# Performance work log

Hardware: AMD Instinct MI355X
Metric: run time of the kernel (lower is better)

Reference implementation:

```python
import jax, jax.numpy as jnp
import numpy as np

NLAG = 300  # int(maxlag/dt) = int(3.0/0.01)


def setup_inputs() -> dict:
    key = jax.random.key(0)
    k1, k2 = jax.random.split(key)
    data1 = jax.random.normal(k1, (64, 32, 3000), dtype=jnp.float32)
    data2 = jax.random.normal(k2, (64, 32, 3000), dtype=jnp.float32)
    return {"data1": data1, "data2": data2}


def reference(data1, data2):
    # Time-domain full cross-correlation via grouped conv1d (PyTorch conv1d
    # does correlation, no kernel flip; lax.conv_general_dilated matches).
    nb, nc, nt = data1.shape
    g = nb * nc
    lhs = data1.reshape(1, g, nt)          # (N=1, C=g, T)
    rhs = data2.reshape(g, 1, nt)          # (O=g, I=1, T) one filter per group
    xcor = jax.lax.conv_general_dilated(
        lhs, rhs,
        window_strides=(1,),
        padding=[(NLAG + 1, NLAG + 1)],
        feature_group_count=g,
        dimension_numbers=("NCH", "OIH", "NCH"),
    )  # (1, g, 2*NLAG+3)
    return xcor.reshape(nb, nc, -1)
```

## Files before the change

### kernel.cpp

```cpp
#include <hip/hip_runtime.h>


#define NT    3000
#define NOUT  603
#define CHPB  4
#define BLOCK 256

#define L1B  6784
#define L2B  8192
#define CHB  (L1B + L2B)
#define TOTB (CHB * CHPB)

typedef short bf16x8 __attribute__((ext_vector_type(8)));
typedef float f32x4  __attribute__((ext_vector_type(4)));

static __device__ __forceinline__ uint f2bf(float f) {
    union { float f; uint u; } a; a.f = f;
    return (a.u + 0x7fffu + ((a.u >> 16) & 1u)) >> 16;
}

__global__ __launch_bounds__(BLOCK, 2) void xcorr_mfma(
    const float* __restrict__ d1g, const float* __restrict__ d2g,
    float* __restrict__ out)
{
    __shared__ __align__(16) unsigned char smem[TOTB];
    const int tid = threadIdx.x;

    int4* z = (int4*)smem;
    for (int i = tid; i < TOTB / 16; i += BLOCK) z[i] = int4{0, 0, 0, 0};
    __syncthreads();

    const int chBase = blockIdx.x * CHPB;

    for (int i = tid; i < CHPB * 750; i += BLOCK) {
        const int c = i / 750, j = i % 750;
        const float4 v = *(const float4*)(d1g + (size_t)(chBase + c) * NT + 4 * j);
        uint2 p;
        p.x = f2bf(v.x) | (f2bf(v.y) << 16);
        p.y = f2bf(v.z) | (f2bf(v.w) << 16);
        *(uint2*)(smem + c * CHB + 608 + 8 * j) = p;
    }
    for (int i = tid; i < CHPB * 750; i += BLOCK) {
        const int c = i / 750, j = i % 750;
        const float4 v = *(const float4*)(d2g + (size_t)(chBase + c) * NT + 4 * j);
        uint2 p;
        p.x = f2bf(v.x) | (f2bf(v.y) << 16);
        p.y = f2bf(v.z) | (f2bf(v.w) << 16);
        *(uint2*)(smem + c * CHB + L1B + 1536 + 8 * j) = p;
    }
    __syncthreads();

    const int wid = tid >> 6, lane = tid & 63;
    const int q = lane >> 4, r = lane & 15;
    const uint* lA = (const uint*)(smem + wid * CHB);
    const uint* lB = (const uint*)(smem + wid * CHB + L1B);

    f32x4 a00 = {0.f,0.f,0.f,0.f};
    f32x4 a10 = {0.f,0.f,0.f,0.f};
    f32x4 a01 = {0.f,0.f,0.f,0.f};
    f32x4 a11 = {0.f,0.f,0.f,0.f};

    int da = 128 + 4 * q + r + 2;
    int db = 384 + 128 + 4 * q - 16 * r;

    #pragma unroll 4
    for (int i = 0; i < 96; ++i) {
        const uint* pa = lA + da;
        const uint Dm1 = pa[-1], D0 = pa[0], D1 = pa[1], D2 = pa[2], D3 = pa[3];

        union { uint u[4]; bf16x8 v; int4 i4; } f1, f0, g0, g1;
        f1.u[0] = D0; f1.u[1] = D1; f1.u[2] = D2; f1.u[3] = D3;
        f0.u[0] = (Dm1 >> 16) | (D0 << 16);
        f0.u[1] = (D0  >> 16) | (D1 << 16);
        f0.u[2] = (D1  >> 16) | (D2 << 16);
        f0.u[3] = (D2  >> 16) | (D3 << 16);
        g0.i4 = *(const int4*)(lB + db);
        g1.i4 = *(const int4*)(lB + db - 256);

        a00 = __builtin_amdgcn_mfma_f32_16x16x32_bf16(f0.v, g0.v, a00, 0, 0, 0);
        a10 = __builtin_amdgcn_mfma_f32_16x16x32_bf16(f1.v, g0.v, a10, 0, 0, 0);
        a01 = __builtin_amdgcn_mfma_f32_16x16x32_bf16(f0.v, g1.v, a01, 0, 0, 0);
        a11 = __builtin_amdgcn_mfma_f32_16x16x32_bf16(f1.v, g1.v, a11, 0, 0, 0);

        da += 16; db += 16;
    }

    float* o = out + (size_t)(chBase + wid) * NOUT;
    {
        const int X = 32 * r + 8 * q;
        float4 s0 = {a00[0], a10[0], a00[1], a10[1]};
        float4 s1 = {a00[2], a10[2], a00[3], a10[3]};
        *(float4*)(o + X)     = s0;
        *(float4*)(o + X + 4) = s1;
    }
    {
        const int X = 512 + 32 * r + 8 * q;
        if (X + 7 < NOUT) {
            float4 s0 = {a01[0], a11[0], a01[1], a11[1]};
            float4 s1 = {a01[2], a11[2], a01[3], a11[3]};
            *(float4*)(o + X)     = s0;
            *(float4*)(o + X + 4) = s1;
        } else if (X < NOUT) {
            const float v[8] = {a01[0], a11[0], a01[1], a11[1],
                                a01[2], a11[2], a01[3], a11[3]};
            #pragma unroll
            for (int e = 0; e < 8; ++e)
                if (X + e < NOUT) o[X + e] = v[e];
        }
    }
}

extern "C" void kernel_launch(void* const* d_in, const int* in_sizes, int n_in,
                              void* d_out, int out_size, void* d_ws, size_t ws_size,
                              hipStream_t stream) {
    const float* d1 = (const float*)d_in[0];
    const float* d2 = (const float*)d_in[1];
    float* out = (float*)d_out;
    const int nChannels = in_sizes[0] / NT;
    const int grid = nChannels / CHPB;
    xcorr_mfma<<<grid, BLOCK, 0, stream>>>(d1, d2, out);
}
```

Baseline: 26.18 us.

## Zero only padding regions and reuse B fragments via register FIFO

```diff
diff --git a/kernel.cpp b/kernel.cpp
--- a/kernel.cpp
+++ b/kernel.cpp
@@ -25,12 +25,18 @@
 {
     __shared__ __align__(16) unsigned char smem[TOTB];
     const int tid = threadIdx.x;
+    const int chBase = blockIdx.x * CHPB;
 
-    int4* z = (int4*)smem;
-    for (int i = tid; i < TOTB / 16; i += BLOCK) z[i] = int4{0, 0, 0, 0};
-    __syncthreads();
-
-    const int chBase = blockIdx.x * CHPB;
+    for (int i = tid; i < CHPB * 196; i += BLOCK) {
+        const int c = i / 196, j = i % 196;
+        const int dw = (j < 152) ? j : (1652 + (j - 152));
+        ((uint*)(smem + c * CHB))[dw] = 0u;
+    }
+    for (int i = tid; i < CHPB * 548; i += BLOCK) {
+        const int c = i / 548, j = i % 548;
+        const int dw = (j < 384) ? j : (1884 + (j - 384));
+        ((uint*)(smem + c * CHB + L1B))[dw] = 0u;
+    }
 
     for (int i = tid; i < CHPB * 750; i += BLOCK) {
         const int c = i / 750, j = i % 750;
@@ -60,29 +66,41 @@
     f32x4 a01 = {0.f,0.f,0.f,0.f};
     f32x4 a11 = {0.f,0.f,0.f,0.f};
 
-    int da = 128 + 4 * q + r + 2;
-    int db = 384 + 128 + 4 * q - 16 * r;
+    int4 fifo[16];
+    {
+        const int dbP = 256 + 4 * q - 16 * r;
+        #pragma unroll
+        for (int s = 0; s < 16; ++s)
+            fifo[s] = *(const int4*)(lB + dbP + 16 * s);
+    }
 
-    #pragma unroll 4
-    for (int i = 0; i < 96; ++i) {
-        const uint* pa = lA + da;
-        const uint Dm1 = pa[-1], D0 = pa[0], D1 = pa[1], D2 = pa[2], D3 = pa[3];
+    int da = 130 + 4 * q + r;
+    int db = 512 + 4 * q - 16 * r;
 
-        union { uint u[4]; bf16x8 v; int4 i4; } f1, f0, g0, g1;
-        f1.u[0] = D0; f1.u[1] = D1; f1.u[2] = D2; f1.u[3] = D3;
-        f0.u[0] = (Dm1 >> 16) | (D0 << 16);
-        f0.u[1] = (D0  >> 16) | (D1 << 16);
-        f0.u[2] = (D1  >> 16) | (D2 << 16);
-        f0.u[3] = (D2  >> 16) | (D3 << 16);
-        g0.i4 = *(const int4*)(lB + db);
-        g1.i4 = *(const int4*)(lB + db - 256);
+    for (int jo = 0; jo < 6; ++jo) {
+        #pragma unroll
+        for (int u = 0; u < 16; ++u) {
+            const uint* pa = lA + da;
+            const uint Dm1 = pa[-1], D0 = pa[0], D1 = pa[1], D2 = pa[2], D3 = pa[3];
 
-        a00 = __builtin_amdgcn_mfma_f32_16x16x32_bf16(f0.v, g0.v, a00, 0, 0, 0);
-        a10 = __builtin_amdgcn_mfma_f32_16x16x32_bf16(f1.v, g0.v, a10, 0, 0, 0);
-        a01 = __builtin_amdgcn_mfma_f32_16x16x32_bf16(f0.v, g1.v, a01, 0, 0, 0);
-        a11 = __builtin_amdgcn_mfma_f32_16x16x32_bf16(f1.v, g1.v, a11, 0, 0, 0);
+            union { uint w[4]; bf16x8 v; int4 i4; } f1, f0, g0, g1;
+            f1.w[0] = D0; f1.w[1] = D1; f1.w[2] = D2; f1.w[3] = D3;
+            f0.w[0] = (Dm1 >> 16) | (D0 << 16);
+            f0.w[1] = (D0  >> 16) | (D1 << 16);
+            f0.w[2] = (D1  >> 16) | (D2 << 16);
+            f0.w[3] = (D2  >> 16) | (D3 << 16);
 
-        da += 16; db += 16;
+            g0.i4 = *(const int4*)(lB + db);
+            g1.i4 = fifo[u];
+            fifo[u] = g0.i4;
+
+            a00 = __builtin_amdgcn_mfma_f32_16x16x32_bf16(f0.v, g0.v, a00, 0, 0, 0);
+            a10 = __builtin_amdgcn_mfma_f32_16x16x32_bf16(f1.v, g0.v, a10, 0, 0, 0);
+            a01 = __builtin_amdgcn_mfma_f32_16x16x32_bf16(f0.v, g1.v, a01, 0, 0, 0);
+            a11 = __builtin_amdgcn_mfma_f32_16x16x32_bf16(f1.v, g1.v, a11, 0, 0, 0);
+
+            da += 16; db += 16;
+        }
     }
 
     float* o = out + (size_t)(chBase + wid) * NOUT;
```

New measurement: 25.69 us. Within noise of the previous version (-1.9%).
